# Kernel tuning notes

Hardware: AMD Instinct MI355X
Metric: run time of the kernel (lower is better)

The kernel has to match this reference:

```python
import jax, jax.numpy as jnp
import numpy as np

EMBED_DIM = 1024
NUM_HEADS = 16
HEAD_DIM = EMBED_DIM // NUM_HEADS
SCALING = HEAD_DIM ** -0.5
T, B = 1024, 4


def setup_inputs() -> dict:
    key = jax.random.key(0)
    k1, k2, k3, k4 = jax.random.split(key, 4)
    x_TBC = jax.random.normal(k1, (T, B, EMBED_DIM), dtype=jnp.float32)
    key_padding_mask = jnp.zeros((B, T), dtype=bool)
    edge_bias = jax.random.normal(k2, (B, NUM_HEADS, T, T), dtype=jnp.float32)
    # xavier_uniform-ish init for weights
    lim_qkv = (6.0 / (EMBED_DIM + 3 * EMBED_DIM)) ** 0.5 / (2 ** 0.5)
    w_qkv = jax.random.uniform(k3, (3 * EMBED_DIM, EMBED_DIM), minval=-lim_qkv, maxval=lim_qkv, dtype=jnp.float32)
    b_qkv = jnp.zeros((3 * EMBED_DIM,), dtype=jnp.float32)
    lim_p = (6.0 / (2 * EMBED_DIM)) ** 0.5
    w_proj = jax.random.uniform(k4, (EMBED_DIM, EMBED_DIM), minval=-lim_p, maxval=lim_p, dtype=jnp.float32)
    b_proj = jnp.zeros((EMBED_DIM,), dtype=jnp.float32)
    return {"x_TBC": x_TBC, "key_padding_mask": key_padding_mask, "edge_bias": edge_bias,
            "w_qkv": w_qkv, "b_qkv": b_qkv, "w_proj": w_proj, "b_proj": b_proj}


def reference(x_TBC, key_padding_mask, edge_bias, w_qkv, b_qkv, w_proj, b_proj):
    Tn, Bn, C = x_TBC.shape
    H, Dh = NUM_HEADS, HEAD_DIM
    qkv = x_TBC @ w_qkv.T + b_qkv               # [T,B,3C]
    q, k, v = jnp.split(qkv, 3, axis=-1)
    def split_heads(t):  # [T,B,C] -> [B,H,T,Dh]
        return t.reshape(Tn, Bn, H, Dh).transpose(1, 2, 0, 3)
    q = split_heads(q) * SCALING
    k = split_heads(k)
    v = split_heads(v)
    logits = jnp.einsum('bhtd,bhsd->bhts', q, k) + edge_bias  # [B,H,T,T]
    neg_inf = jnp.finfo(logits.dtype).min
    logits = jnp.where(key_padding_mask[:, None, None, :], neg_inf, logits)
    attn = jax.nn.softmax(logits, axis=-1)
    out = jnp.einsum('bhts,bhsd->bhtd', attn, v)  # [B,H,T,Dh]
    out = out.transpose(2, 0, 1, 3).reshape(Tn, Bn, C)  # [T,B,C]
    out = out @ w_proj.T + b_proj
    return out
```

## Files before the change

### kernel.cpp

```cpp
#include <hip/hip_runtime.h>
#include <stdint.h>
#include <math.h>

#define TT  1024
#define BBN 4
#define CCH 1024
#define HHN 16
#define DHD 64
#define MMR 4096
#define N3  3072

typedef __attribute__((ext_vector_type(4))) float  f32x4;
typedef __attribute__((ext_vector_type(8))) short  s16x8;
typedef __attribute__((ext_vector_type(8))) __bf16 bf16x8;

static __device__ __forceinline__ f32x4 mfma16(s16x8 a, s16x8 b, f32x4 c) {
  return __builtin_amdgcn_mfma_f32_16x16x32_bf16(
      __builtin_bit_cast(bf16x8, a), __builtin_bit_cast(bf16x8, b), c, 0, 0, 0);
}

static __device__ __forceinline__ unsigned short f2bf(float f) {
  union { float f; unsigned int u; } v; v.f = f;
  unsigned int u = v.u;
  return (unsigned short)((u + 0x7FFFu + ((u >> 16) & 1u)) >> 16);
}

typedef const __attribute__((address_space(1))) void GVoid;
typedef __attribute__((address_space(3))) void LVoid;
static __device__ __forceinline__ void gll16(const void* g, void* l) {
  __builtin_amdgcn_global_load_lds((GVoid*)g, (LVoid*)l, 16, 0, 0);
}

#if __has_builtin(__builtin_amdgcn_exp2f)
#define EXP2F(x) __builtin_amdgcn_exp2f(x)
#else
#define EXP2F(x) exp2f(x)
#endif

__global__ void cvt_all(const float* __restrict__ x, const float* __restrict__ wqkv,
                        const float* __restrict__ wproj, unsigned short* __restrict__ out) {
  int i = blockIdx.x * blockDim.x + threadIdx.x;
  const float4* src;
  int off;
  if (i < 1048576)      { src = (const float4*)x;     off = 0; }
  else if (i < 1835008) { src = (const float4*)wqkv;  off = 1048576; }
  else                  { src = (const float4*)wproj; off = 1835008; }
  float4 f = src[i - off];
  ushort4 o;
  o.x = f2bf(f.x); o.y = f2bf(f.y); o.z = f2bf(f.z); o.w = f2bf(f.w);
  ((ushort4*)out)[i] = o;
}

template <int MODE, int BN>
__global__ __launch_bounds__(256, MODE == 0 ? 4 : 3) void gemm_bt(
    const unsigned short* __restrict__ A, const unsigned short* __restrict__ Bw,
    const float* __restrict__ bias, float* __restrict__ Cout,
    unsigned short* __restrict__ qb, unsigned short* __restrict__ kb,
    unsigned short* __restrict__ vtb, int M, int N, int K) {
  constexpr int NI = BN / 32;
  constexpr int AH = 128 * 32;
  constexpr int BH = BN * 32;
  __shared__ __align__(16) unsigned short sMem[2 * AH + 2 * BH];
  unsigned short* sA0 = sMem;
  unsigned short* sB0 = sMem + 2 * AH;
  const int tid = threadIdx.x;
  const int l = tid & 63, w = tid >> 6;
  const int g = l >> 4, c = l & 15;
  const int wr = w >> 1, wc = w & 1;
  const int total = gridDim.x * gridDim.y;
  const int flat = blockIdx.y * gridDim.x + blockIdx.x;
  const int wg = (flat & 7) * (total >> 3) + (flat >> 3);
  const int bxs = wg % gridDim.x, bys = wg / gridDim.x;
  const int bm = bys * 128, bn = bxs * BN;

  const int srow = w * 16 + (l >> 2);
  const int schG = (l & 3) ^ ((l >> 3) & 3);
  const unsigned short* Agp = A + (size_t)(bm + srow) * K + schG * 8;
  const unsigned short* Bgp = Bw + (size_t)(bn + srow) * K + schG * 8;
  const int swzR = (c >> 1) & 3;

  f32x4 acc[4][NI] = {};

#define GSTAGE(s, h) do {                                                        \
    _Pragma("unroll")                                                            \
    for (int i_ = 0; i_ < 2; ++i_)                                               \
      gll16(Agp + (size_t)(i_ * 64) * K + (s) * 32,                              \
            sA0 + (h) * AH + i_ * 2048 + w * 512);                               \
    _Pragma("unroll")                                                            \
    for (int i_ = 0; i_ < BN / 64; ++i_)                                         \
      gll16(Bgp + (size_t)(i_ * 64) * K + (s) * 32,                              \
            sB0 + (h) * BH + i_ * 2048 + w * 512);                               \
  } while (0)

#define GWAITN do {                                                              \
    if constexpr (BN == 128) asm volatile("s_waitcnt vmcnt(4)" ::: "memory");    \
    else                     asm volatile("s_waitcnt vmcnt(3)" ::: "memory");    \
  } while (0)

  const int NS = K >> 5;
  GSTAGE(0, 0);
  GSTAGE(1, 1);
  GWAITN;
  __builtin_amdgcn_s_barrier();

#pragma unroll 1
  for (int s = 0;; ++s) {
    const int h = s & 1;
    s16x8 af[4], bfr[NI];
#pragma unroll
    for (int mi = 0; mi < 4; ++mi)
      af[mi] = *(const s16x8*)&sA0[h * AH + (wr * 64 + mi * 16 + c) * 32 + (g ^ swzR) * 8];
#pragma unroll
    for (int ni = 0; ni < NI; ++ni)
      bfr[ni] = *(const s16x8*)&sB0[h * BH + (wc * (BN / 2) + ni * 16 + c) * 32 + (g ^ swzR) * 8];
#pragma unroll
    for (int mi = 0; mi < 4; ++mi)
#pragma unroll
      for (int ni = 0; ni < NI; ++ni)
        acc[mi][ni] = mfma16(af[mi], bfr[ni], acc[mi][ni]);
    if (s == NS - 1) break;
    __builtin_amdgcn_s_barrier();
    if (s + 2 < NS) { GSTAGE(s + 2, h); GWAITN; }
    else            { asm volatile("s_waitcnt vmcnt(0)" ::: "memory"); }
    __builtin_amdgcn_s_barrier();
  }

#undef GSTAGE
#undef GWAITN

  if (MODE == 1 && (bn >> 10) == 2) {
    unsigned short* sT = sMem;
    const int tl0 = bm >> 2;
#pragma unroll
    for (int pc = 0; pc < 2; ++pc) {
      __syncthreads();
      if (wc == pc) {
#pragma unroll
        for (int mi = 0; mi < 4; ++mi)
#pragma unroll
          for (int ni = 0; ni < NI; ++ni) {
            const int col = bn + pc * 64 + ni * 16 + c;
            const float bsv = bias[col];
#pragma unroll
            for (int j = 0; j < 4; ++j)
              sT[(wr * 64 + mi * 16 + g * 4 + j) * 72 + ni * 16 + c] =
                  f2bf(acc[mi][ni][j] + bsv);
          }
      }
      __syncthreads();
      const int h2 = ((bn + pc * 64) & 1023) >> 6;
      unsigned short* vdst = vtb + ((size_t)(w * 16 + h2) * 64 + l) * 1024 + tl0;
#pragma unroll
      for (int q8 = 0; q8 < 4; ++q8) {
        unsigned short pk[8];
#pragma unroll
        for (int e = 0; e < 8; ++e)
          pk[e] = sT[(((q8 * 8 + e) << 2) | w) * 72 + l];
        *(s16x8*)&vdst[q8 * 8] = *(const s16x8*)pk;
      }
    }
    return;
  }

#pragma unroll
  for (int mi = 0; mi < 4; ++mi)
#pragma unroll
    for (int ni = 0; ni < NI; ++ni) {
      const int col = bn + wc * (BN / 2) + ni * 16 + c;
      const float bsv = bias[col];
      if (MODE == 0) {
#pragma unroll
        for (int j = 0; j < 4; ++j) {
          const int r = bm + wr * 64 + mi * 16 + g * 4 + j;
          Cout[(size_t)r * N + col] = acc[mi][ni][j] + bsv;
        }
      } else {
        const int rem = col & 1023;
        const int h = rem >> 6, d = rem & 63;
        const bool isq = (col >> 10) == 0;
        const float qscale = 0.18033688f;
#pragma unroll
        for (int j = 0; j < 4; ++j) {
          const int r = bm + wr * 64 + mi * 16 + g * 4 + j;
          const int t = r >> 2, bb = r & 3;
          const int bh = bb * 16 + h;
          float av = acc[mi][ni][j] + bsv;
          if (isq) qb[((size_t)bh * 1024 + t) * 64 + d] = f2bf(av * qscale);
          else     kb[((size_t)bh * 1024 + t) * 64 + d] = f2bf(av);
        }
      }
    }
}

__global__ __launch_bounds__(256, 3) void attn_kernel(
    const unsigned short* __restrict__ qb, const unsigned short* __restrict__ kb,
    const unsigned short* __restrict__ vtb, const float* __restrict__ eb,
    const unsigned char* __restrict__ mask, unsigned short* __restrict__ ob) {
  __shared__ __align__(16) unsigned short sQ[64 * 64];
  __shared__ __align__(16) unsigned short sK[2][64 * 64];
  __shared__ __align__(16) unsigned short sV[2][64 * 64];
  __shared__ __align__(16) unsigned short sP[4][16 * 72];
  __shared__ __align__(4) unsigned char sM[1024];
  const int tid = threadIdx.x;
  const int l = tid & 63, w = tid >> 6;
  const int g = l >> 4, c = l & 15;
  const int flat = blockIdx.y * 16 + blockIdx.x;
  const int wg = (flat & 7) * 128 + (flat >> 3);
  const int q0 = (wg & 15) * 64;
  const int bh = wg >> 4;
  const int b = bh >> 4;
  const int srow = tid >> 3, sch = tid & 7;

  const unsigned short* qg = qb + (size_t)bh * 65536;
  const unsigned short* kg = kb + (size_t)bh * 65536;
  const unsigned short* vg = vtb + (size_t)bh * 65536;
  const float* ebg = eb + (size_t)bh * 1048576 + (size_t)(q0 + w * 16 + g * 4) * 1024;

  const float BS = 1.44269504f;
  float bvA[4][4], bvB[4][4];
  float ps[4] = {0.f, 0.f, 0.f, 0.f};
  f32x4 po[4] = {};

#define STAGE(tv, P) do {                                                        \
    _Pragma("unroll")                                                            \
    for (int i_ = 0; i_ < 2; ++i_) {                                             \
      int row_ = i_ * 32 + srow;                                                 \
      gll16(kg + (size_t)((tv) * 64 + row_) * 64 + (sch ^ (row_ & 7)) * 8,       \
            &sK[P][i_ * 2048 + w * 512]);                                        \
      gll16(vg + (size_t)row_ * 1024 + (tv) * 64 + (sch ^ (row_ & 7)) * 8,       \
            &sV[P][i_ * 2048 + w * 512]);                                        \
    } } while (0)

#define BIAS(tv, BV) do {                                                        \
    _Pragma("unroll")                                                            \
    for (int ni_ = 0; ni_ < 4; ++ni_)                                            \
      _Pragma("unroll")                                                          \
      for (int j_ = 0; j_ < 4; ++j_)                                             \
        BV[ni_][j_] = ebg[(size_t)j_ * 1024 + (tv) * 64 + ni_ * 16 + c];         \
    } while (0)

#define TILE(P, BV, s0v) do {                                                    \
    float mkc_[4];                                                               \
    _Pragma("unroll")                                                            \
    for (int ni_ = 0; ni_ < 4; ++ni_)                                            \
      mkc_[ni_] = sM[(s0v) + ni_ * 16 + c] ? -1e30f : -8.0f;                     \
    s16x8 kf_[4][2];                                                             \
    _Pragma("unroll")                                                            \
    for (int ni_ = 0; ni_ < 4; ++ni_)                                            \
      _Pragma("unroll")                                                          \
      for (int k2_ = 0; k2_ < 2; ++k2_) {                                        \
        int row_ = ni_ * 16 + c;                                                 \
        kf_[ni_][k2_] = *(const s16x8*)&sK[P][row_ * 64 +                        \
                         (((k2_ * 4 + g) ^ (row_ & 7)) * 8)];                    \
      }                                                                          \
    f32x4 sc_[4] = {};                                                           \
    _Pragma("unroll")                                                            \
    for (int k2_ = 0; k2_ < 2; ++k2_)                                            \
      _Pragma("unroll")                                                          \
      for (int ni_ = 0; ni_ < 4; ++ni_)                                          \
        sc_[ni_] = mfma16(qf[k2_], kf_[ni_][k2_], sc_[ni_]);                     \
    _Pragma("unroll")                                                            \
    for (int ni_ = 0; ni_ < 4; ++ni_)                                            \
      _Pragma("unroll")                                                          \
      for (int j_ = 0; j_ < 4; ++j_) {                                           \
        float x_ = fmaf(BV[ni_][j_], BS, sc_[ni_][j_]) + mkc_[ni_];              \
        float p_ = EXP2F(x_);                                                    \
        sP[w][(g * 4 + j_) * 72 + ni_ * 16 + c] = f2bf(p_);                      \
        ps[j_] += p_;                                                            \
      }                                                                          \
    s16x8 vf_[4][2];                                                             \
    _Pragma("unroll")                                                            \
    for (int nd_ = 0; nd_ < 4; ++nd_)                                            \
      _Pragma("unroll")                                                          \
      for (int k2_ = 0; k2_ < 2; ++k2_) {                                        \
        int row_ = nd_ * 16 + c;                                                 \
        vf_[nd_][k2_] = *(const s16x8*)&sV[P][row_ * 64 +                        \
                         (((k2_ * 4 + g) ^ (row_ & 7)) * 8)];                    \
      }                                                                          \
    asm volatile("s_waitcnt lgkmcnt(0)" ::: "memory");                           \
    __builtin_amdgcn_sched_barrier(0);                                           \
    s16x8 pf_[2];                                                                \
    _Pragma("unroll")                                                            \
    for (int k2_ = 0; k2_ < 2; ++k2_)                                            \
      pf_[k2_] = *(const s16x8*)&sP[w][c * 72 + k2_ * 32 + g * 8];               \
    _Pragma("unroll")                                                            \
    for (int k2_ = 0; k2_ < 2; ++k2_)                                            \
      _Pragma("unroll")                                                          \
      for (int nd_ = 0; nd_ < 4; ++nd_)                                          \
        po[nd_] = mfma16(pf_[k2_], vf_[nd_][k2_], po[nd_]);                      \
  } while (0)

#pragma unroll
  for (int i = 0; i < 2; ++i) {
    int row = i * 32 + srow;
    gll16(qg + (size_t)(q0 + row) * 64 + (sch ^ (row & 7)) * 8, &sQ[i * 2048 + w * 512]);
  }
  STAGE(0, 0);
  STAGE(1, 1);
  BIAS(0, bvA);
  BIAS(1, bvB);
  ((unsigned int*)sM)[tid] = ((const unsigned int*)(mask + b * TT))[tid & 255];
  __syncthreads();

  s16x8 qf[2];
#pragma unroll
  for (int kk2 = 0; kk2 < 2; ++kk2) {
    int row = w * 16 + c;
    qf[kk2] = *(const s16x8*)&sQ[row * 64 + (((kk2 * 4 + g) ^ (row & 7)) * 8)];
  }

#pragma unroll 1
  for (int t2 = 0;; t2 += 2) {
    TILE(0, bvA, t2 * 64);
    __builtin_amdgcn_s_barrier();
    if (t2 + 2 < 16) { STAGE(t2 + 2, 0); BIAS(t2 + 2, bvA); }
    if (t2 == 14) { asm volatile("s_waitcnt vmcnt(16)" ::: "memory"); }
    else          { asm volatile("s_waitcnt vmcnt(36)" ::: "memory"); }
    __builtin_amdgcn_s_barrier();
    TILE(1, bvB, t2 * 64 + 64);
    if (t2 == 14) break;
    __builtin_amdgcn_s_barrier();
    STAGE(t2 + 3, 1); BIAS(t2 + 3, bvB);
    asm volatile("s_waitcnt vmcnt(36)" ::: "memory");
    __builtin_amdgcn_s_barrier();
  }

#undef STAGE
#undef BIAS
#undef TILE

#pragma unroll
  for (int j = 0; j < 4; ++j) {
#pragma unroll
    for (int off = 1; off <= 8; off <<= 1)
      ps[j] += __shfl_xor(ps[j], off, 64);
    ps[j] = 1.0f / ps[j];
  }
  const int h = bh & 15;
#pragma unroll
  for (int nd = 0; nd < 4; ++nd)
#pragma unroll
    for (int j = 0; j < 4; ++j) {
      float val = po[nd][j] * ps[j];
      int t = q0 + w * 16 + g * 4 + j;
      ob[((size_t)t * 4 + b) * 1024 + h * 64 + nd * 16 + c] = f2bf(val);
    }
}

extern "C" void kernel_launch(void* const* d_in, const int* in_sizes, int n_in,
                              void* d_out, int out_size, void* d_ws, size_t ws_size,
                              hipStream_t stream) {
  const float* x      = (const float*)d_in[0];
  const unsigned char* mask = (const unsigned char*)d_in[1];
  const float* ebias  = (const float*)d_in[2];
  const float* wqkv   = (const float*)d_in[3];
  const float* bqkv   = (const float*)d_in[4];
  const float* wproj  = (const float*)d_in[5];
  const float* bproj  = (const float*)d_in[6];
  float* out = (float*)d_out;

  char* ws = (char*)d_ws;
  unsigned short* xb    = (unsigned short*)(ws);
  unsigned short* wqkvb = (unsigned short*)(ws + 8388608);
  unsigned short* wpb   = (unsigned short*)(ws + 14680064);
  unsigned short* qbuf  = (unsigned short*)(ws + 16777216);
  unsigned short* kbuf  = (unsigned short*)(ws + 25165824);
  unsigned short* vtbuf = (unsigned short*)(ws + 33554432);
  unsigned short* obuf  = (unsigned short*)(ws + 41943040);

  cvt_all<<<8192, 256, 0, stream>>>(x, wqkv, wproj, xb);

  gemm_bt<1, 128><<<dim3(24, 32), 256, 0, stream>>>(
      xb, wqkvb, bqkv, nullptr, qbuf, kbuf, vtbuf, MMR, N3, 1024);

  attn_kernel<<<dim3(16, 64), 256, 0, stream>>>(
      qbuf, kbuf, vtbuf, ebias, mask, obuf);

  gemm_bt<0, 64><<<dim3(16, 32), 256, 0, stream>>>(
      obuf, wpb, bproj, out, nullptr, nullptr, nullptr, MMR, 1024, 1024);
}
```

Before: 147.4 us.

## Halve attention KV tile to 32 keys and load Q fragments directly

The attention kernel now stages 32-key K/V tiles instead of 64 and shrinks the per-wave P buffer. Q fragments are read straight from global memory into registers, so the Q shared buffer is gone. Both changes cut LDS use and registers so the launch bound can target 4 blocks per SM instead of 3. In exchange the key loop runs twice as many iterations with more barriers, the bias prefetch per stage is smaller, and the vmcnt wait counts and swizzle patterns are retuned.

```diff
diff --git a/kernel.cpp b/kernel.cpp
--- a/kernel.cpp
+++ b/kernel.cpp
@@ -192,14 +192,13 @@
     }
 }
 
-__global__ __launch_bounds__(256, 3) void attn_kernel(
+__global__ __launch_bounds__(256, 4) void attn_kernel(
     const unsigned short* __restrict__ qb, const unsigned short* __restrict__ kb,
     const unsigned short* __restrict__ vtb, const float* __restrict__ eb,
     const unsigned char* __restrict__ mask, unsigned short* __restrict__ ob) {
-  __shared__ __align__(16) unsigned short sQ[64 * 64];
-  __shared__ __align__(16) unsigned short sK[2][64 * 64];
-  __shared__ __align__(16) unsigned short sV[2][64 * 64];
-  __shared__ __align__(16) unsigned short sP[4][16 * 72];
+  __shared__ __align__(16) unsigned short sK[2][32 * 64];
+  __shared__ __align__(16) unsigned short sV[2][64 * 32];
+  __shared__ __align__(16) unsigned short sP[4][16 * 40];
   __shared__ __align__(4) unsigned char sM[1024];
   const int tid = threadIdx.x;
   const int l = tid & 63, w = tid >> 6;
@@ -209,7 +208,8 @@
   const int q0 = (wg & 15) * 64;
   const int bh = wg >> 4;
   const int b = bh >> 4;
-  const int srow = tid >> 3, sch = tid & 7;
+  const int srK = w * 8 + (l >> 3), scK = l & 7;
+  const int srV = w * 16 + (l >> 2), scV = l & 3;
 
   const unsigned short* qg = qb + (size_t)bh * 65536;
   const unsigned short* kg = kb + (size_t)bh * 65536;
@@ -217,84 +217,69 @@
   const float* ebg = eb + (size_t)bh * 1048576 + (size_t)(q0 + w * 16 + g * 4) * 1024;
 
   const float BS = 1.44269504f;
-  float bvA[4][4], bvB[4][4];
+  float bvA[2][4], bvB[2][4];
   float ps[4] = {0.f, 0.f, 0.f, 0.f};
   f32x4 po[4] = {};
 
 #define STAGE(tv, P) do {                                                        \
-    _Pragma("unroll")                                                            \
-    for (int i_ = 0; i_ < 2; ++i_) {                                             \
-      int row_ = i_ * 32 + srow;                                                 \
-      gll16(kg + (size_t)((tv) * 64 + row_) * 64 + (sch ^ (row_ & 7)) * 8,       \
-            &sK[P][i_ * 2048 + w * 512]);                                        \
-      gll16(vg + (size_t)row_ * 1024 + (tv) * 64 + (sch ^ (row_ & 7)) * 8,       \
-            &sV[P][i_ * 2048 + w * 512]);                                        \
-    } } while (0)
+    gll16(kg + (size_t)((tv) * 32 + srK) * 64 + ((scK ^ (srK & 7)) * 8),         \
+          &sK[P][w * 512]);                                                      \
+    gll16(vg + (size_t)srV * 1024 + (tv) * 32 + ((scV ^ ((srV >> 1) & 3)) * 8),  \
+          &sV[P][w * 512]);                                                      \
+  } while (0)
 
 #define BIAS(tv, BV) do {                                                        \
     _Pragma("unroll")                                                            \
-    for (int ni_ = 0; ni_ < 4; ++ni_)                                            \
+    for (int ni_ = 0; ni_ < 2; ++ni_)                                            \
       _Pragma("unroll")                                                          \
       for (int j_ = 0; j_ < 4; ++j_)                                             \
-        BV[ni_][j_] = ebg[(size_t)j_ * 1024 + (tv) * 64 + ni_ * 16 + c];         \
+        BV[ni_][j_] = ebg[(size_t)j_ * 1024 + (tv) * 32 + ni_ * 16 + c];         \
     } while (0)
 
 #define TILE(P, BV, s0v) do {                                                    \
-    float mkc_[4];                                                               \
-    _Pragma("unroll")                                                            \
-    for (int ni_ = 0; ni_ < 4; ++ni_)                                            \
+    float mkc_[2];                                                               \
+    _Pragma("unroll")                                                            \
+    for (int ni_ = 0; ni_ < 2; ++ni_)                                            \
       mkc_[ni_] = sM[(s0v) + ni_ * 16 + c] ? -1e30f : -8.0f;                     \
-    s16x8 kf_[4][2];                                                             \
-    _Pragma("unroll")                                                            \
-    for (int ni_ = 0; ni_ < 4; ++ni_)                                            \
+    s16x8 kf_[2][2];                                                             \
+    _Pragma("unroll")                                                            \
+    for (int ni_ = 0; ni_ < 2; ++ni_)                                            \
       _Pragma("unroll")                                                          \
-      for (int k2_ = 0; k2_ < 2; ++k2_) {                                        \
-        int row_ = ni_ * 16 + c;                                                 \
-        kf_[ni_][k2_] = *(const s16x8*)&sK[P][row_ * 64 +                        \
-                         (((k2_ * 4 + g) ^ (row_ & 7)) * 8)];                    \
-      }                                                                          \
-    f32x4 sc_[4] = {};                                                           \
+      for (int k2_ = 0; k2_ < 2; ++k2_)                                          \
+        kf_[ni_][k2_] = *(const s16x8*)&sK[P][(ni_ * 16 + c) * 64 +              \
+                         (((k2_ * 4 + g) ^ (c & 7)) * 8)];                       \
+    f32x4 sc_[2] = {};                                                           \
     _Pragma("unroll")                                                            \
     for (int k2_ = 0; k2_ < 2; ++k2_)                                            \
       _Pragma("unroll")                                                          \
-      for (int ni_ = 0; ni_ < 4; ++ni_)                                          \
+      for (int ni_ = 0; ni_ < 2; ++ni_)                                          \
         sc_[ni_] = mfma16(qf[k2_], kf_[ni_][k2_], sc_[ni_]);                     \
     _Pragma("unroll")                                                            \
-    for (int ni_ = 0; ni_ < 4; ++ni_)                                            \
+    for (int ni_ = 0; ni_ < 2; ++ni_)                                            \
       _Pragma("unroll")                                                          \
       for (int j_ = 0; j_ < 4; ++j_) {                                           \
         float x_ = fmaf(BV[ni_][j_], BS, sc_[ni_][j_]) + mkc_[ni_];              \
         float p_ = EXP2F(x_);                                                    \
-        sP[w][(g * 4 + j_) * 72 + ni_ * 16 + c] = f2bf(p_);                      \
+        sP[w][(g * 4 + j_) * 40 + ni_ * 16 + c] = f2bf(p_);                      \
         ps[j_] += p_;                                                            \
       }                                                                          \
-    s16x8 vf_[4][2];                                                             \
+    s16x8 vf_[4];                                                                \
     _Pragma("unroll")                                                            \
     for (int nd_ = 0; nd_ < 4; ++nd_)                                            \
-      _Pragma("unroll")                                                          \
-      for (int k2_ = 0; k2_ < 2; ++k2_) {                                        \
-        int row_ = nd_ * 16 + c;                                                 \
-        vf_[nd_][k2_] = *(const s16x8*)&sV[P][row_ * 64 +                        \
-                         (((k2_ * 4 + g) ^ (row_ & 7)) * 8)];                    \
-      }                                                                          \
+      vf_[nd_] = *(const s16x8*)&sV[P][(nd_ * 16 + c) * 32 +                     \
+                  ((g ^ ((c >> 1) & 3)) * 8)];                                   \
     asm volatile("s_waitcnt lgkmcnt(0)" ::: "memory");                           \
     __builtin_amdgcn_sched_barrier(0);                                           \
-    s16x8 pf_[2];                                                                \
-    _Pragma("unroll")                                                            \
-    for (int k2_ = 0; k2_ < 2; ++k2_)                                            \
-      pf_[k2_] = *(const s16x8*)&sP[w][c * 72 + k2_ * 32 + g * 8];               \
-    _Pragma("unroll")                                                            \
-    for (int k2_ = 0; k2_ < 2; ++k2_)                                            \
-      _Pragma("unroll")                                                          \
-      for (int nd_ = 0; nd_ < 4; ++nd_)                                          \
-        po[nd_] = mfma16(pf_[k2_], vf_[nd_][k2_], po[nd_]);                      \
+    s16x8 pf_ = *(const s16x8*)&sP[w][c * 40 + g * 8];                           \
+    _Pragma("unroll")                                                            \
+    for (int nd_ = 0; nd_ < 4; ++nd_)                                            \
+      po[nd_] = mfma16(pf_, vf_[nd_], po[nd_]);                                  \
   } while (0)
 
-#pragma unroll
-  for (int i = 0; i < 2; ++i) {
-    int row = i * 32 + srow;
-    gll16(qg + (size_t)(q0 + row) * 64 + (sch ^ (row & 7)) * 8, &sQ[i * 2048 + w * 512]);
-  }
+  s16x8 qf[2];
+#pragma unroll
+  for (int kk2 = 0; kk2 < 2; ++kk2)
+    qf[kk2] = *(const s16x8*)&qg[(size_t)(q0 + w * 16 + c) * 64 + kk2 * 32 + g * 8];
   STAGE(0, 0);
   STAGE(1, 1);
   BIAS(0, bvA);
@@ -302,26 +287,22 @@
   ((unsigned int*)sM)[tid] = ((const unsigned int*)(mask + b * TT))[tid & 255];
   __syncthreads();
 
-  s16x8 qf[2];
-#pragma unroll
-  for (int kk2 = 0; kk2 < 2; ++kk2) {
-    int row = w * 16 + c;
-    qf[kk2] = *(const s16x8*)&sQ[row * 64 + (((kk2 * 4 + g) ^ (row & 7)) * 8)];
-  }
-
 #pragma unroll 1
   for (int t2 = 0;; t2 += 2) {
-    TILE(0, bvA, t2 * 64);
-    __builtin_amdgcn_s_barrier();
-    if (t2 + 2 < 16) { STAGE(t2 + 2, 0); BIAS(t2 + 2, bvA); }
-    if (t2 == 14) { asm volatile("s_waitcnt vmcnt(16)" ::: "memory"); }
-    else          { asm volatile("s_waitcnt vmcnt(36)" ::: "memory"); }
-    __builtin_amdgcn_s_barrier();
-    TILE(1, bvB, t2 * 64 + 64);
-    if (t2 == 14) break;
+    TILE(0, bvA, t2 * 32);
+    __builtin_amdgcn_s_barrier();
+    if (t2 + 2 < 32) {
+      STAGE(t2 + 2, 0); BIAS(t2 + 2, bvA);
+      asm volatile("s_waitcnt vmcnt(10)" ::: "memory");
+    } else {
+      asm volatile("s_waitcnt vmcnt(0)" ::: "memory");
+    }
+    __builtin_amdgcn_s_barrier();
+    TILE(1, bvB, t2 * 32 + 32);
+    if (t2 == 30) break;
     __builtin_amdgcn_s_barrier();
     STAGE(t2 + 3, 1); BIAS(t2 + 3, bvB);
-    asm volatile("s_waitcnt vmcnt(36)" ::: "memory");
+    asm volatile("s_waitcnt vmcnt(10)" ::: "memory");
     __builtin_amdgcn_s_barrier();
   }
 
```

After: 148.8 us. No clear change (+1.0%).
